# Optimization experiments

Measured on AMD Instinct MI355X. Metric: run time of the kernel, lower is better.

The kernel has to match this reference:

```python
import jax, jax.numpy as jnp
import numpy as np

B, D, E, H, DEPTH, NH, K = 4, 384, 8, 1536, 12, 6, 2
P, NTOK = 16, 197  # patch size, 14*14 patches + cls
EPS = 1e-6


def layernorm(x, w, b):
    m = x.mean(-1, keepdims=True)
    v = ((x - m) ** 2).mean(-1, keepdims=True)
    return (x - m) / jnp.sqrt(v + EPS) * w + b


def attention(x, qkv_w, qkv_b, proj_w, proj_b):
    Bn, N, C = x.shape
    hd = C // NH
    qkv = x @ qkv_w.T + qkv_b                       # [B,N,3C]
    qkv = qkv.reshape(Bn, N, 3, NH, hd).transpose(2, 0, 3, 1, 4)
    q, k, v = qkv[0], qkv[1], qkv[2]                # [B,h,N,hd]
    attn = jax.nn.softmax((q @ k.transpose(0, 1, 3, 2)) * (hd ** -0.5), axis=-1)
    out = (attn @ v).transpose(0, 2, 1, 3).reshape(Bn, N, C)
    return out @ proj_w.T + proj_b


def mlp(x, w1, b1, w2, b2):
    h = jax.nn.gelu(x @ w1.T + b1, approximate=False)
    return h @ w2.T + b2


def moe_ffn(x2d, gw, w1, b1, w2, b2):
    # noiseless top-k gating (eval mode of NoisyTopKGating)
    logits = x2d @ gw                                # [T,E]
    T = logits.shape[0]
    top_vals, top_idx = jax.lax.top_k(logits, K + 1)
    gates_k = jax.nn.softmax(top_vals[:, :K], axis=-1)
    gates = jnp.zeros((T, E), x2d.dtype).at[jnp.arange(T)[:, None], top_idx[:, :K]].set(gates_k)
    # dense per-expert FFN, weighted combine (identical math to SparseDispatcher)
    h = jax.nn.gelu(jnp.einsum('td,edh->teh', x2d, w1) + b1, approximate=False)
    out = jnp.einsum('teh,ehd->ted', h, w2) + b2
    return jnp.einsum('te,ted->td', gates, out)


def forward(x, patch_w, patch_b, cls_token, pos_embed,
            ln1_w, ln1_b, qkv_w, qkv_b, proj_w, proj_b, ln2_w, ln2_b,
            fc1_w, fc1_b, fc2_w, fc2_b,
            gate_w, moe_w1, moe_b1, moe_w2, moe_b2, lnf_w, lnf_b):
    # patch embed: conv k=16 s=16
    feat = jax.lax.conv_general_dilated(x, patch_w, (P, P), 'VALID',
                                        dimension_numbers=('NCHW', 'OIHW', 'NCHW'))
    feat = feat + patch_b[None, :, None, None]
    Bn = feat.shape[0]
    tokens = feat.reshape(Bn, D, -1).transpose(0, 2, 1)          # [B,196,D]
    cls = jnp.broadcast_to(cls_token, (Bn, 1, D))
    h = jnp.concatenate([cls, tokens], axis=1) + pos_embed       # [B,197,D]

    for i in range(DEPTH):
        h = h + attention(layernorm(h, ln1_w[i], ln1_b[i]), qkv_w[i], qkv_b[i], proj_w[i], proj_b[i])
        y = layernorm(h, ln2_w[i], ln2_b[i])
        if i % 2 == 1:
            j = i // 2
            y2 = moe_ffn(y.reshape(-1, D), gate_w[j], moe_w1[j], moe_b1[j], moe_w2[j], moe_b2[j])
            h = h + y2.reshape(Bn, NTOK, D)
        else:
            j = i // 2
            h = h + mlp(y, fc1_w[j], fc1_b[j], fc2_w[j], fc2_b[j])
    return layernorm(h, lnf_w, lnf_b)


def setup_inputs() -> dict:
    key = jax.random.key(0)
    ks = jax.random.split(key, 16)
    rn = lambda k, s, sd=0.02: jax.random.normal(k, s, jnp.float32) * sd
    return {
        'x': jax.random.normal(ks[0], (B, 3, 224, 224), jnp.float32),
        'patch_w': rn(ks[1], (D, 3, P, P)), 'patch_b': jnp.zeros((D,), jnp.float32),
        'cls_token': rn(ks[2], (1, 1, D)), 'pos_embed': rn(ks[3], (1, NTOK, D)),
        'ln1_w': jnp.ones((DEPTH, D), jnp.float32), 'ln1_b': jnp.zeros((DEPTH, D), jnp.float32),
        'qkv_w': rn(ks[4], (DEPTH, 3 * D, D)), 'qkv_b': jnp.zeros((DEPTH, 3 * D), jnp.float32),
        'proj_w': rn(ks[5], (DEPTH, D, D)), 'proj_b': jnp.zeros((DEPTH, D), jnp.float32),
        'ln2_w': jnp.ones((DEPTH, D), jnp.float32), 'ln2_b': jnp.zeros((DEPTH, D), jnp.float32),
        'fc1_w': rn(ks[6], (DEPTH // 2, H, D)), 'fc1_b': jnp.zeros((DEPTH // 2, H), jnp.float32),
        'fc2_w': rn(ks[7], (DEPTH // 2, D, H)), 'fc2_b': jnp.zeros((DEPTH // 2, D), jnp.float32),
        'gate_w': rn(ks[8], (DEPTH // 2, D, E)),
        'moe_w1': rn(ks[9], (DEPTH // 2, E, D, H)), 'moe_b1': jnp.zeros((DEPTH // 2, E, H), jnp.float32),
        'moe_w2': rn(ks[10], (DEPTH // 2, E, H, D)), 'moe_b2': jnp.zeros((DEPTH // 2, E, D), jnp.float32),
        'lnf_w': jnp.ones((D,), jnp.float32), 'lnf_b': jnp.zeros((D,), jnp.float32),
    }


def reference(x, patch_w, patch_b, cls_token, pos_embed,
              ln1_w, ln1_b, qkv_w, qkv_b, proj_w, proj_b, ln2_w, ln2_b,
              fc1_w, fc1_b, fc2_w, fc2_b,
              gate_w, moe_w1, moe_b1, moe_w2, moe_b2, lnf_w, lnf_b):
    return forward(x, patch_w, patch_b, cls_token, pos_embed,
                   ln1_w, ln1_b, qkv_w, qkv_b, proj_w, proj_b, ln2_w, ln2_b,
                   fc1_w, fc1_b, fc2_w, fc2_b,
                   gate_w, moe_w1, moe_b1, moe_w2, moe_b2, lnf_w, lnf_b)
```

## Files before the change

### kernel.cpp

```cpp
#include <hip/hip_runtime.h>
#include <math.h>

#define NBATCH 4
#define NTOK 197
#define TT 788
#define DM 384
#define HM 1536
#define NHEAD 6
#define NEXP 8
#define LD2 72

typedef __attribute__((ext_vector_type(8))) short bf16x8;
typedef __attribute__((ext_vector_type(4))) float f32x4;

__device__ __forceinline__ void f2bf2(float x, short& hi, short& lo) {
    unsigned u = __float_as_uint(x);
    unsigned uh = u + (0x7fffu + ((u >> 16) & 1u));
    hi = (short)(uh >> 16);
    float hf = __uint_as_float(uh & 0xffff0000u);
    float r = x - hf;
    unsigned v = __float_as_uint(r);
    lo = (short)((v + (0x7fffu + ((v >> 16) & 1u))) >> 16);
}
__device__ __forceinline__ float gelu_f(float x) {
    return 0.5f * x * (1.0f + erff(x * 0.7071067811865475f));
}

__global__ void k_ln(const float* __restrict__ X, const float* __restrict__ w,
                     const float* __restrict__ b, float* __restrict__ Y) {
    int t = blockIdx.x, lane = threadIdx.x;
    const float* x = X + (size_t)t * DM;
    float v[6];
    float s = 0.f;
    #pragma unroll
    for (int i = 0; i < 6; ++i) { v[i] = x[lane + i * 64]; s += v[i]; }
    #pragma unroll
    for (int off = 32; off; off >>= 1) s += __shfl_xor(s, off);
    float mean = s * (1.f / 384.f);
    float q = 0.f;
    #pragma unroll
    for (int i = 0; i < 6; ++i) { float d = v[i] - mean; q += d * d; }
    #pragma unroll
    for (int off = 32; off; off >>= 1) q += __shfl_xor(q, off);
    float inv = rsqrtf(q * (1.f / 384.f) + 1e-6f);
    float* y = Y + (size_t)t * DM;
    #pragma unroll
    for (int i = 0; i < 6; ++i) {
        int d = lane + i * 64;
        y[d] = (v[i] - mean) * inv * w[d] + b[d];
    }
}

__global__ __launch_bounds__(256) void k_patch_gemm(
    const float* __restrict__ X, const float* __restrict__ W,
    const float* __restrict__ pb, const float* __restrict__ cls,
    const float* __restrict__ pos, float* __restrict__ H)
{
    const int M = 784, N = 384, K = 768, MT = 13, NT = 6;
    int mt, nt;
    {
        int lane8 = blockIdx.x & 7;
        int idx = blockIdx.x >> 3;
        nt = idx % NT;
        mt = lane8 + 8 * (idx / NT);
        if (mt >= MT) return;
    }
    __shared__ short Ah[64 * LD2], Al[64 * LD2], Bh[64 * LD2], Bl[64 * LD2];
    const int bm = mt * 64, bn = nt * 64;
    const int tid = threadIdx.x;
    const int lane = tid & 63, w = tid >> 6;
    const int wr = w >> 1, wc = w & 1;
    const int r16 = lane & 15, g = lane >> 4;
    const int sr = tid >> 4;
    const int sc = (tid & 15) * 4;
    const float* cvb[4];
    bool aok[4];
    #pragma unroll
    for (int p = 0; p < 4; ++p) {
        int row = bm + sr + p * 16;
        aok[p] = row < M;
        int b = row / 196, pp = row % 196;
        int py = pp / 14, px = pp % 14;
        cvb[p] = X + (size_t)b * 150528 + (size_t)(py * 16) * 224 + px * 16;
    }
    float4 ra[4], rb[4];
    auto LOADT = [&](int k0) {
        int k = k0 + sc;
        int c = k >> 8, ii = (k >> 4) & 15, j = k & 15;
        size_t coff = (size_t)c * 50176 + ii * 224 + j;
        #pragma unroll
        for (int p = 0; p < 4; ++p) {
            ra[p] = aok[p] ? *(const float4*)(cvb[p] + coff) : make_float4(0.f, 0.f, 0.f, 0.f);
            rb[p] = *(const float4*)(W + (size_t)(bn + sr + p * 16) * K + k0 + sc);
        }
    };
    auto STORET = [&]() {
        #pragma unroll
        for (int p = 0; p < 4; ++p) {
            int r = sr + p * 16;
            float4 a4 = ra[p], b4 = rb[p];
            short4 ah, al, bh, bl;
            f2bf2(a4.x, ah.x, al.x); f2bf2(a4.y, ah.y, al.y);
            f2bf2(a4.z, ah.z, al.z); f2bf2(a4.w, ah.w, al.w);
            f2bf2(b4.x, bh.x, bl.x); f2bf2(b4.y, bh.y, bl.y);
            f2bf2(b4.z, bh.z, bl.z); f2bf2(b4.w, bh.w, bl.w);
            *(short4*)&Ah[r * LD2 + sc] = ah; *(short4*)&Al[r * LD2 + sc] = al;
            *(short4*)&Bh[r * LD2 + sc] = bh; *(short4*)&Bl[r * LD2 + sc] = bl;
        }
    };
    f32x4 acc[2][2] = {};
    auto COMPUTE = [&]() {
        #pragma unroll
        for (int kk = 0; kk < 2; ++kk) {
            bf16x8 afh[2], afl[2], bfh[2], bfl[2];
            #pragma unroll
            for (int i = 0; i < 2; ++i) {
                int off = (wr * 32 + i * 16 + r16) * LD2 + kk * 32 + g * 8;
                afh[i] = *(const bf16x8*)&Ah[off];
                afl[i] = *(const bf16x8*)&Al[off];
            }
            #pragma unroll
            for (int j = 0; j < 2; ++j) {
                int off = (wc * 32 + j * 16 + r16) * LD2 + kk * 32 + g * 8;
                bfh[j] = *(const bf16x8*)&Bh[off];
                bfl[j] = *(const bf16x8*)&Bl[off];
            }
            #pragma unroll
            for (int i = 0; i < 2; ++i)
                #pragma unroll
                for (int j = 0; j < 2; ++j) {
                    acc[i][j] = __builtin_amdgcn_mfma_f32_16x16x32_bf16(afl[i], bfh[j], acc[i][j], 0, 0, 0);
                    acc[i][j] = __builtin_amdgcn_mfma_f32_16x16x32_bf16(afh[i], bfl[j], acc[i][j], 0, 0, 0);
                    acc[i][j] = __builtin_amdgcn_mfma_f32_16x16x32_bf16(afh[i], bfh[j], acc[i][j], 0, 0, 0);
                }
        }
    };
    LOADT(0);
    STORET();
    __syncthreads();
    for (int k0 = 64; k0 < K; k0 += 64) {
        LOADT(k0);
        COMPUTE();
        __syncthreads();
        STORET();
        __syncthreads();
    }
    COMPUTE();
    #pragma unroll
    for (int i = 0; i < 2; ++i) {
        #pragma unroll
        for (int j = 0; j < 2; ++j) {
            int n = bn + wc * 32 + j * 16 + r16;
            int mbase = bm + wr * 32 + i * 16 + g * 4;
            #pragma unroll
            for (int r = 0; r < 4; ++r) {
                int m = mbase + r;
                if (m < M) {
                    int b = m / 196, pp = m % 196;
                    int t = b * NTOK + 1 + pp;
                    H[(size_t)t * DM + n] = acc[i][j][r] + pb[n] + pos[(size_t)(1 + pp) * DM + n];
                }
            }
        }
    }
    if (blockIdx.x == 0) {
        for (int idx = tid; idx < NBATCH * DM; idx += 256) {
            int b = idx / DM, d = idx % DM;
            H[(size_t)(b * NTOK) * DM + d] = cls[d] + pos[d];
        }
    }
}

__global__ __launch_bounds__(256) void k_gemm_mfma(
    const float* __restrict__ A, const float* __restrict__ W,
    const float* __restrict__ bias, float* __restrict__ C,
    int M, int N, int K, int flags, int MT, int NT, int wprot, int ksplit,
    const float* __restrict__ lnw, const float* __restrict__ lnb)
{
    int mt, nt, ks = 0;
    {
        int lane8 = blockIdx.x & 7;
        int idx = blockIdx.x >> 3;
        if (ksplit > 1) { ks = idx % ksplit; idx /= ksplit; }
        if (wprot) {
            mt = idx % MT;
            nt = lane8 + 8 * (idx / MT);
            if (nt >= NT) return;
        } else {
            nt = idx % NT;
            mt = lane8 + 8 * (idx / NT);
            if (mt >= MT) return;
        }
    }
    const int Ks = K / ksplit;
    const float* Ab = A + (size_t)ks * Ks;
    const float* Wb = W + (size_t)ks * Ks;
    __shared__ short Ah[64 * LD2], Al[64 * LD2], Bh[64 * LD2], Bl[64 * LD2];
    const int bm = mt * 64, bn = nt * 64;
    const int tid = threadIdx.x;
    const int lane = tid & 63, w = tid >> 6;
    const int wr = w >> 1, wc = w & 1;
    const int r16 = lane & 15, g = lane >> 4;
    const int sr = tid >> 4;
    const int sc = (tid & 15) * 4;
    const bool doln = (flags & 8) != 0;
    float am[4], ai[4];
    #pragma unroll
    for (int p = 0; p < 4; ++p) { am[p] = 0.f; ai[p] = 1.f; }
    if (doln) {
        int j = tid & 15;
        #pragma unroll
        for (int p = 0; p < 4; ++p) {
            int r = bm + sr + p * 16;
            if (r < M) {
                const float* xr = A + (size_t)r * K;
                float s = 0.f, ss = 0.f;
                #pragma unroll
                for (int i = 0; i < 6; ++i) {
                    float4 v = *(const float4*)(xr + j * 4 + i * 64);
                    s += v.x + v.y + v.z + v.w;
                    ss += v.x * v.x + v.y * v.y + v.z * v.z + v.w * v.w;
                }
                #pragma unroll
                for (int off = 1; off < 16; off <<= 1) {
                    s += __shfl_xor(s, off);
                    ss += __shfl_xor(ss, off);
                }
                float mean = s * (1.f / 384.f);
                float var = ss * (1.f / 384.f) - mean * mean;
                am[p] = mean;
                ai[p] = rsqrtf(var + 1e-6f);
            }
        }
    }
    float4 ra[4], rb[4], lw4, lb4;
    auto LOADT = [&](int k0) {
        if (doln) {
            lw4 = *(const float4*)(lnw + k0 + sc);
            lb4 = *(const float4*)(lnb + k0 + sc);
        }
        #pragma unroll
        for (int p = 0; p < 4; ++p) {
            int r = sr + p * 16;
            ra[p] = make_float4(0.f, 0.f, 0.f, 0.f);
            if (bm + r < M) ra[p] = *(const float4*)(Ab + (size_t)(bm + r) * K + k0 + sc);
            rb[p] = *(const float4*)(Wb + (size_t)(bn + r) * K + k0 + sc);
        }
    };
    auto STORET = [&]() {
        #pragma unroll
        for (int p = 0; p < 4; ++p) {
            int r = sr + p * 16;
            float4 a4 = ra[p];
            if (doln) {
                a4.x = (a4.x - am[p]) * ai[p] * lw4.x + lb4.x;
                a4.y = (a4.y - am[p]) * ai[p] * lw4.y + lb4.y;
                a4.z = (a4.z - am[p]) * ai[p] * lw4.z + lb4.z;
                a4.w = (a4.w - am[p]) * ai[p] * lw4.w + lb4.w;
            }
            float4 b4 = rb[p];
            short4 ah, al, bh, bl;
            f2bf2(a4.x, ah.x, al.x); f2bf2(a4.y, ah.y, al.y);
            f2bf2(a4.z, ah.z, al.z); f2bf2(a4.w, ah.w, al.w);
            f2bf2(b4.x, bh.x, bl.x); f2bf2(b4.y, bh.y, bl.y);
            f2bf2(b4.z, bh.z, bl.z); f2bf2(b4.w, bh.w, bl.w);
            *(short4*)&Ah[r * LD2 + sc] = ah; *(short4*)&Al[r * LD2 + sc] = al;
            *(short4*)&Bh[r * LD2 + sc] = bh; *(short4*)&Bl[r * LD2 + sc] = bl;
        }
    };
    f32x4 acc[2][2] = {};
    auto COMPUTE = [&]() {
        #pragma unroll
        for (int kk = 0; kk < 2; ++kk) {
            bf16x8 afh[2], afl[2], bfh[2], bfl[2];
            #pragma unroll
            for (int i = 0; i < 2; ++i) {
                int off = (wr * 32 + i * 16 + r16) * LD2 + kk * 32 + g * 8;
                afh[i] = *(const bf16x8*)&Ah[off];
                afl[i] = *(const bf16x8*)&Al[off];
            }
            #pragma unroll
            for (int j = 0; j < 2; ++j) {
                int off = (wc * 32 + j * 16 + r16) * LD2 + kk * 32 + g * 8;
                bfh[j] = *(const bf16x8*)&Bh[off];
                bfl[j] = *(const bf16x8*)&Bl[off];
            }
            #pragma unroll
            for (int i = 0; i < 2; ++i)
                #pragma unroll
                for (int j = 0; j < 2; ++j) {
                    acc[i][j] = __builtin_amdgcn_mfma_f32_16x16x32_bf16(afl[i], bfh[j], acc[i][j], 0, 0, 0);
                    acc[i][j] = __builtin_amdgcn_mfma_f32_16x16x32_bf16(afh[i], bfl[j], acc[i][j], 0, 0, 0);
                    acc[i][j] = __builtin_amdgcn_mfma_f32_16x16x32_bf16(afh[i], bfh[j], acc[i][j], 0, 0, 0);
                }
        }
    };
    LOADT(0);
    STORET();
    __syncthreads();
    for (int k0 = 64; k0 < Ks; k0 += 64) {
        LOADT(k0);
        COMPUTE();
        __syncthreads();
        STORET();
        __syncthreads();
    }
    COMPUTE();
    #pragma unroll
    for (int i = 0; i < 2; ++i) {
        #pragma unroll
        for (int j = 0; j < 2; ++j) {
            int n = bn + wc * 32 + j * 16 + r16;
            float bb = (bias && ks == 0) ? bias[n] : 0.f;
            int mbase = bm + wr * 32 + i * 16 + g * 4;
            #pragma unroll
            for (int r = 0; r < 4; ++r) {
                int m = mbase + r;
                if (m < M) {
                    float v = acc[i][j][r] + bb;
                    float* cp = C + (size_t)m * N + n;
                    if (flags & 16) {
                        atomicAdd(cp, v);
                    } else {
                        if (flags & 1) v = gelu_f(v);
                        if (flags & 2) v += *cp;
                        *cp = v;
                    }
                }
            }
        }
    }
}

__global__ __launch_bounds__(256) void k_scoresm(const float* __restrict__ QKV,
                                                 float* __restrict__ S) {
    int z = blockIdx.y;
    int b = z / NHEAD, hh = z % NHEAD;
    int i0 = blockIdx.x * 32;
    __shared__ float qs[32][65];
    __shared__ float ks[32][65];
    __shared__ float srow[32][200];
    int tid = threadIdx.x;
    int r = tid >> 3, d0 = (tid & 7) * 8, c0 = (tid & 7) * 4, l8 = tid & 7;
    {
        float4 v0 = make_float4(0,0,0,0), v1 = v0;
        if (i0 + r < NTOK) {
            const float* qp = QKV + ((size_t)(b * NTOK + i0 + r)) * 1152 + hh * 64 + d0;
            v0 = *(const float4*)qp; v1 = *(const float4*)(qp + 4);
        }
        qs[r][d0+0]=v0.x; qs[r][d0+1]=v0.y; qs[r][d0+2]=v0.z; qs[r][d0+3]=v0.w;
        qs[r][d0+4]=v1.x; qs[r][d0+5]=v1.y; qs[r][d0+6]=v1.z; qs[r][d0+7]=v1.w;
    }
    if (l8 == 0) { srow[r][197] = -1e30f; srow[r][198] = -1e30f; srow[r][199] = -1e30f; }
    for (int j0 = 0; j0 < NTOK; j0 += 32) {
        __syncthreads();
        {
            float4 v0 = make_float4(0,0,0,0), v1 = v0;
            if (j0 + r < NTOK) {
                const float* kp = QKV + ((size_t)(b * NTOK + j0 + r)) * 1152 + 384 + hh * 64 + d0;
                v0 = *(const float4*)kp; v1 = *(const float4*)(kp + 4);
            }
            ks[r][d0+0]=v0.x; ks[r][d0+1]=v0.y; ks[r][d0+2]=v0.z; ks[r][d0+3]=v0.w;
            ks[r][d0+4]=v1.x; ks[r][d0+5]=v1.y; ks[r][d0+6]=v1.z; ks[r][d0+7]=v1.w;
        }
        __syncthreads();
        float acc[4] = {0.f, 0.f, 0.f, 0.f};
        #pragma unroll 8
        for (int d = 0; d < 64; ++d) {
            float qv = qs[r][d];
            #pragma unroll
            for (int u = 0; u < 4; ++u) acc[u] += qv * ks[c0 + u][d];
        }
        #pragma unroll
        for (int u = 0; u < 4; ++u) {
            int j = j0 + c0 + u;
            if (j < NTOK) srow[r][j] = acc[u] * 0.125f;
        }
    }
    __syncthreads();
    float m = -1e30f;
    for (int c = l8; c < 200; c += 8) m = fmaxf(m, srow[r][c]);
    #pragma unroll
    for (int off = 1; off < 8; off <<= 1) m = fmaxf(m, __shfl_xor(m, off));
    float s = 0.f;
    for (int c = l8; c < 200; c += 8) {
        float e = expf(srow[r][c] - m);
        srow[r][c] = e;
        s += e;
    }
    #pragma unroll
    for (int off = 1; off < 8; off <<= 1) s += __shfl_xor(s, off);
    float invs = 1.f / s;
    int i = i0 + r;
    if (i < NTOK) {
        float* sp = S + ((size_t)z * NTOK + i) * NTOK;
        for (int c = l8; c < NTOK; c += 8) sp[c] = srow[r][c] * invs;
    }
}

__global__ __launch_bounds__(256) void k_pv(const float* __restrict__ S, const float* __restrict__ QKV,
                                            float* __restrict__ AO) {
    int z = blockIdx.y;
    int b = z / NHEAD, hh = z % NHEAD;
    int i0 = blockIdx.x * 32;
    __shared__ float ps[32][33];
    __shared__ float vs[32][65];
    int tid = threadIdx.x;
    int r = tid >> 3;
    int c4 = (tid & 7) * 4;
    int d0 = (tid & 7) * 8;
    float acc[8] = {};
    for (int k0 = 0; k0 < NTOK; k0 += 32) {
        #pragma unroll
        for (int u = 0; u < 4; ++u) {
            int i = i0 + r, j = k0 + c4 + u;
            ps[r][c4 + u] = (i < NTOK && j < NTOK) ? S[((size_t)z * NTOK + i) * NTOK + j] : 0.f;
        }
        {
            float4 v0 = make_float4(0,0,0,0), v1 = v0;
            if (k0 + r < NTOK) {
                const float* vp = QKV + ((size_t)(b * NTOK + k0 + r)) * 1152 + 768 + hh * 64 + d0;
                v0 = *(const float4*)vp; v1 = *(const float4*)(vp + 4);
            }
            vs[r][d0+0]=v0.x; vs[r][d0+1]=v0.y; vs[r][d0+2]=v0.z; vs[r][d0+3]=v0.w;
            vs[r][d0+4]=v1.x; vs[r][d0+5]=v1.y; vs[r][d0+6]=v1.z; vs[r][d0+7]=v1.w;
        }
        __syncthreads();
        #pragma unroll 8
        for (int kk = 0; kk < 32; ++kk) {
            float pw = ps[r][kk];
            #pragma unroll
            for (int j = 0; j < 8; ++j) acc[j] += pw * vs[kk][d0 + j];
        }
        __syncthreads();
    }
    int i = i0 + r;
    if (i < NTOK) {
        float* op = AO + (size_t)(b * NTOK + i) * DM + hh * 64 + d0;
        #pragma unroll
        for (int j = 0; j < 8; ++j) op[j] = acc[j];
    }
}

__global__ void k_route_ln(const float* __restrict__ H, float* __restrict__ lnstat,
                           const float* __restrict__ lnw, const float* __restrict__ lnb,
                           const float* __restrict__ GW,
                           int* __restrict__ eidx, float* __restrict__ egate) {
    int t = blockIdx.x * 4 + (threadIdx.x >> 6);
    if (t >= TT) return;
    int lane = threadIdx.x & 63;
    const float* x = H + (size_t)t * DM;
    float v[6];
    float s = 0.f, ss = 0.f;
    #pragma unroll
    for (int i = 0; i < 6; ++i) {
        v[i] = x[lane + i * 64];
        s += v[i];
        ss += v[i] * v[i];
    }
    #pragma unroll
    for (int off = 32; off; off >>= 1) { s += __shfl_xor(s, off); ss += __shfl_xor(ss, off); }
    float mean = s * (1.f / 384.f);
    float var = ss * (1.f / 384.f) - mean * mean;
    float inv = rsqrtf(var + 1e-6f);
    if (lane == 0) { lnstat[2 * t] = mean; lnstat[2 * t + 1] = inv; }
    float l8v[NEXP] = {};
    #pragma unroll
    for (int i = 0; i < 6; ++i) {
        int d = lane + i * 64;
        float yv = (v[i] - mean) * inv * lnw[d] + lnb[d];
        const float* g = GW + (size_t)d * NEXP;
        #pragma unroll
        for (int e = 0; e < NEXP; ++e) l8v[e] += yv * g[e];
    }
    #pragma unroll
    for (int e = 0; e < NEXP; ++e) {
        float vv = l8v[e];
        #pragma unroll
        for (int off = 32; off; off >>= 1) vv += __shfl_xor(vv, off);
        l8v[e] = vv;
    }
    if (lane == 0) {
        int b0 = 0;
        #pragma unroll
        for (int e = 1; e < NEXP; ++e) if (l8v[e] > l8v[b0]) b0 = e;
        int b1 = -1;
        #pragma unroll
        for (int e = 0; e < NEXP; ++e) if (e != b0 && (b1 < 0 || l8v[e] > l8v[b1])) b1 = e;
        float e1 = expf(l8v[b1] - l8v[b0]);
        float denom = 1.f + e1;
        eidx[2 * t] = b0; eidx[2 * t + 1] = b1;
        egate[2 * t] = 1.f / denom; egate[2 * t + 1] = e1 / denom;
    }
}

__global__ void k_pscatter(int* __restrict__ cnt, int* __restrict__ basep,
                           const int* __restrict__ eidx, const float* __restrict__ egate,
                           int* __restrict__ slot_tok, float* __restrict__ slot_gate) {
    __shared__ int hist[NEXP];
    __shared__ int bp[NEXP];
    __shared__ int fl[NEXP];
    int tid = threadIdx.x;
    if (tid < NEXP) { hist[tid] = 0; fl[tid] = 0; }
    __syncthreads();
    for (int i = tid; i < 2 * TT; i += 256) atomicAdd(&hist[eidx[i]], 1);
    __syncthreads();
    if (tid == 0) {
        int s = 0;
        for (int e = 0; e < NEXP; ++e) { bp[e] = s; s += hist[e]; }
    }
    __syncthreads();
    if (tid < NEXP) { cnt[tid] = hist[tid]; basep[tid] = bp[tid]; }
    for (int t = tid; t < TT; t += 256) {
        #pragma unroll
        for (int k = 0; k < 2; ++k) {
            int e = eidx[2 * t + k];
            int pos = atomicAdd(&fl[e], 1);
            int s = bp[e] + pos;
            slot_tok[s] = t;
            slot_gate[s] = egate[2 * t + k];
        }
    }
}

__global__ __launch_bounds__(256) void k_moe1_mfma(
    const float* __restrict__ H, const float* __restrict__ lnstat,
    const float* __restrict__ lnw, const float* __restrict__ lnb,
    const float* __restrict__ W1, const float* __restrict__ B1,
    const int* __restrict__ slot_tok, const int* __restrict__ cnt, const int* __restrict__ basep,
    float* __restrict__ HID)
{
    const int e = blockIdx.x & 7;
    const int idx = blockIdx.x >> 3;
    const int mt = idx % 13;
    const int nt = idx / 13;
    const int c = cnt[e];
    const int r0 = mt * 64;
    if (r0 >= c) return;
    const int sbase = basep[e];
    const int n0 = nt * 64;
    const float* W = W1 + (size_t)e * DM * HM;
    const float* B1e = B1 + (size_t)e * HM;
    __shared__ short Ah[64 * LD2], Al[64 * LD2], Bh[64 * LD2], Bl[64 * LD2];
    const int tid = threadIdx.x;
    const int lane = tid & 63, w = tid >> 6;
    const int wr = w >> 1, wc = w & 1;
    const int r16 = lane & 15, g = lane >> 4;
    const int sr = tid >> 4, sc = (tid & 15) * 4;
    const int kq = (tid >> 4) * 4;
    int tokp[4];
    float am4[4], ai4[4];
    #pragma unroll
    for (int p = 0; p < 4; ++p) {
        int m = r0 + sr + p * 16;
        tokp[p] = (m < c) ? slot_tok[sbase + m] : -1;
        am4[p] = 0.f; ai4[p] = 1.f;
        if (tokp[p] >= 0) { am4[p] = lnstat[2 * tokp[p]]; ai4[p] = lnstat[2 * tokp[p] + 1]; }
    }
    f32x4 acc[2][2] = {};
    for (int k0 = 0; k0 < DM; k0 += 64) {
        float4 lw4 = *(const float4*)(lnw + k0 + sc);
        float4 lb4 = *(const float4*)(lnb + k0 + sc);
        #pragma unroll
        for (int p = 0; p < 4; ++p) {
            int r = sr + p * 16;
            float4 a4 = make_float4(0.f, 0.f, 0.f, 0.f);
            if (tokp[p] >= 0) {
                a4 = *(const float4*)(H + (size_t)tokp[p] * DM + k0 + sc);
                a4.x = (a4.x - am4[p]) * ai4[p] * lw4.x + lb4.x;
                a4.y = (a4.y - am4[p]) * ai4[p] * lw4.y + lb4.y;
                a4.z = (a4.z - am4[p]) * ai4[p] * lw4.z + lb4.z;
                a4.w = (a4.w - am4[p]) * ai4[p] * lw4.w + lb4.w;
            }
            short4 ah, al;
            f2bf2(a4.x, ah.x, al.x); f2bf2(a4.y, ah.y, al.y);
            f2bf2(a4.z, ah.z, al.z); f2bf2(a4.w, ah.w, al.w);
            *(short4*)&Ah[r * LD2 + sc] = ah; *(short4*)&Al[r * LD2 + sc] = al;
        }
        {
            float4 b4[4];
            #pragma unroll
            for (int i = 0; i < 4; ++i)
                b4[i] = *(const float4*)(W + (size_t)(k0 + kq + i) * HM + n0 + sc);
            float col[4][4] = {
                { b4[0].x, b4[1].x, b4[2].x, b4[3].x },
                { b4[0].y, b4[1].y, b4[2].y, b4[3].y },
                { b4[0].z, b4[1].z, b4[2].z, b4[3].z },
                { b4[0].w, b4[1].w, b4[2].w, b4[3].w } };
            #pragma unroll
            for (int u = 0; u < 4; ++u) {
                short4 hh, ll;
                f2bf2(col[u][0], hh.x, ll.x); f2bf2(col[u][1], hh.y, ll.y);
                f2bf2(col[u][2], hh.z, ll.z); f2bf2(col[u][3], hh.w, ll.w);
                *(short4*)&Bh[(sc + u) * LD2 + kq] = hh;
                *(short4*)&Bl[(sc + u) * LD2 + kq] = ll;
            }
        }
        __syncthreads();
        #pragma unroll
        for (int kk = 0; kk < 2; ++kk) {
            bf16x8 afh[2], afl[2], bfh[2], bfl[2];
            #pragma unroll
            for (int i = 0; i < 2; ++i) {
                int off = (wr * 32 + i * 16 + r16) * LD2 + kk * 32 + g * 8;
                afh[i] = *(const bf16x8*)&Ah[off];
                afl[i] = *(const bf16x8*)&Al[off];
            }
            #pragma unroll
            for (int j = 0; j < 2; ++j) {
                int off = (wc * 32 + j * 16 + r16) * LD2 + kk * 32 + g * 8;
                bfh[j] = *(const bf16x8*)&Bh[off];
                bfl[j] = *(const bf16x8*)&Bl[off];
            }
            #pragma unroll
            for (int i = 0; i < 2; ++i)
                #pragma unroll
                for (int j = 0; j < 2; ++j) {
                    acc[i][j] = __builtin_amdgcn_mfma_f32_16x16x32_bf16(afl[i], bfh[j], acc[i][j], 0, 0, 0);
                    acc[i][j] = __builtin_amdgcn_mfma_f32_16x16x32_bf16(afh[i], bfl[j], acc[i][j], 0, 0, 0);
                    acc[i][j] = __builtin_amdgcn_mfma_f32_16x16x32_bf16(afh[i], bfh[j], acc[i][j], 0, 0, 0);
                }
        }
        __syncthreads();
    }
    #pragma unroll
    for (int i = 0; i < 2; ++i) {
        #pragma unroll
        for (int j = 0; j < 2; ++j) {
            int n = n0 + wc * 32 + j * 16 + r16;
            float bb = B1e[n];
            #pragma unroll
            for (int r = 0; r < 4; ++r) {
                int m = r0 + wr * 32 + i * 16 + g * 4 + r;
                if (m < c)
                    HID[(size_t)(sbase + m) * HM + n] = gelu_f(acc[i][j][r] + bb);
            }
        }
    }
}

__global__ __launch_bounds__(256) void k_moe2_mfma(
    const float* __restrict__ HID, const float* __restrict__ W2, const float* __restrict__ B2,
    const int* __restrict__ cnt, const int* __restrict__ basep,
    const int* __restrict__ slot_tok, const float* __restrict__ slot_gate,
    float* __restrict__ H)
{
    const int e = blockIdx.x & 7;
    const int idx = blockIdx.x >> 3;
    const int mt = idx % 13;
    const int rest = idx / 13;
    const int nt = rest % 6;
    const int ks = rest / 6;
    const int c = cnt[e];
    const int r0 = mt * 64;
    if (r0 >= c) return;
    const int sbase = basep[e];
    const int n0 = nt * 64;
    const int kbase = ks * 384;
    const float* W = W2 + (size_t)e * HM * DM + (size_t)kbase * DM;
    const float* B2e = B2 + (size_t)e * DM;
    __shared__ short Ah[64 * LD2], Al[64 * LD2], Bh[64 * LD2], Bl[64 * LD2];
    const int tid = threadIdx.x;
    const int lane = tid & 63, w = tid >> 6;
    const int wr = w >> 1, wc = w & 1;
    const int r16 = lane & 15, g = lane >> 4;
    const int sr = tid >> 4, sc = (tid & 15) * 4;
    const int kq = (tid >> 4) * 4;
    f32x4 acc[2][2] = {};
    for (int k0 = 0; k0 < 384; k0 += 64) {
        #pragma unroll
        for (int p = 0; p < 4; ++p) {
            int r = sr + p * 16;
            int m = r0 + r;
            float4 a4 = make_float4(0.f, 0.f, 0.f, 0.f);
            if (m < c) a4 = *(const float4*)(HID + (size_t)(sbase + m) * HM + kbase + k0 + sc);
            short4 ah, al;
            f2bf2(a4.x, ah.x, al.x); f2bf2(a4.y, ah.y, al.y);
            f2bf2(a4.z, ah.z, al.z); f2bf2(a4.w, ah.w, al.w);
            *(short4*)&Ah[r * LD2 + sc] = ah; *(short4*)&Al[r * LD2 + sc] = al;
        }
        {
            float4 b4[4];
            #pragma unroll
            for (int i = 0; i < 4; ++i)
                b4[i] = *(const float4*)(W + (size_t)(k0 + kq + i) * DM + n0 + sc);
            float col[4][4] = {
                { b4[0].x, b4[1].x, b4[2].x, b4[3].x },
                { b4[0].y, b4[1].y, b4[2].y, b4[3].y },
                { b4[0].z, b4[1].z, b4[2].z, b4[3].z },
                { b4[0].w, b4[1].w, b4[2].w, b4[3].w } };
            #pragma unroll
            for (int u = 0; u < 4; ++u) {
                short4 hh, ll;
                f2bf2(col[u][0], hh.x, ll.x); f2bf2(col[u][1], hh.y, ll.y);
                f2bf2(col[u][2], hh.z, ll.z); f2bf2(col[u][3], hh.w, ll.w);
                *(short4*)&Bh[(sc + u) * LD2 + kq] = hh;
                *(short4*)&Bl[(sc + u) * LD2 + kq] = ll;
            }
        }
        __syncthreads();
        #pragma unroll
        for (int kk = 0; kk < 2; ++kk) {
            bf16x8 afh[2], afl[2], bfh[2], bfl[2];
            #pragma unroll
            for (int i = 0; i < 2; ++i) {
                int off = (wr * 32 + i * 16 + r16) * LD2 + kk * 32 + g * 8;
                afh[i] = *(const bf16x8*)&Ah[off];
                afl[i] = *(const bf16x8*)&Al[off];
            }
            #pragma unroll
            for (int j = 0; j < 2; ++j) {
                int off = (wc * 32 + j * 16 + r16) * LD2 + kk * 32 + g * 8;
                bfh[j] = *(const bf16x8*)&Bh[off];
                bfl[j] = *(const bf16x8*)&Bl[off];
            }
            #pragma unroll
            for (int i = 0; i < 2; ++i)
                #pragma unroll
                for (int j = 0; j < 2; ++j) {
                    acc[i][j] = __builtin_amdgcn_mfma_f32_16x16x32_bf16(afl[i], bfh[j], acc[i][j], 0, 0, 0);
                    acc[i][j] = __builtin_amdgcn_mfma_f32_16x16x32_bf16(afh[i], bfl[j], acc[i][j], 0, 0, 0);
                    acc[i][j] = __builtin_amdgcn_mfma_f32_16x16x32_bf16(afh[i], bfh[j], acc[i][j], 0, 0, 0);
                }
        }
        __syncthreads();
    }
    #pragma unroll
    for (int i = 0; i < 2; ++i) {
        #pragma unroll
        for (int j = 0; j < 2; ++j) {
            int n = n0 + wc * 32 + j * 16 + r16;
            float bb = (ks == 0) ? B2e[n] : 0.f;
            #pragma unroll
            for (int r = 0; r < 4; ++r) {
                int m = r0 + wr * 32 + i * 16 + g * 4 + r;
                if (m < c) {
                    int tok = slot_tok[sbase + m];
                    float gt = slot_gate[sbase + m];
                    atomicAdd(&H[(size_t)tok * DM + n], gt * (acc[i][j][r] + bb));
                }
            }
        }
    }
}

extern "C" void kernel_launch(void* const* d_in, const int* in_sizes, int n_in,
                              void* d_out, int out_size, void* d_ws, size_t ws_size,
                              hipStream_t stream) {
    const float* x         = (const float*)d_in[0];
    const float* patch_w   = (const float*)d_in[1];
    const float* patch_b   = (const float*)d_in[2];
    const float* cls_token = (const float*)d_in[3];
    const float* pos_embed = (const float*)d_in[4];
    const float* ln1_w     = (const float*)d_in[5];
    const float* ln1_b     = (const float*)d_in[6];
    const float* qkv_w     = (const float*)d_in[7];
    const float* qkv_b     = (const float*)d_in[8];
    const float* proj_w    = (const float*)d_in[9];
    const float* proj_b    = (const float*)d_in[10];
    const float* ln2_w     = (const float*)d_in[11];
    const float* ln2_b     = (const float*)d_in[12];
    const float* fc1_w     = (const float*)d_in[13];
    const float* fc1_b     = (const float*)d_in[14];
    const float* fc2_w     = (const float*)d_in[15];
    const float* fc2_b     = (const float*)d_in[16];
    const float* gate_w    = (const float*)d_in[17];
    const float* moe_w1    = (const float*)d_in[18];
    const float* moe_b1    = (const float*)d_in[19];
    const float* moe_w2    = (const float*)d_in[20];
    const float* moe_b2    = (const float*)d_in[21];
    const float* lnf_w     = (const float*)d_in[22];
    const float* lnf_b     = (const float*)d_in[23];
    float* out = (float*)d_out;

    float* wsf = (float*)d_ws;
    float* regA     = wsf;
    float* moehid   = regA;
    float* h     = regA + 2420736;
    float* spare = h + 302592;
    float* qkvb  = spare + 302592;
    float* attno = qkvb + 907776;
    float* regC  = attno + 302592;
    float* S    = regC;
    float* hid  = regC;
    float* egate = regC + 1210368;
    int* ib       = (int*)(egate + 1576);
    int* eidx     = ib;
    int* slot_tok = ib + 1576;
    int* slot_of  = ib + 3152;
    int* cnt      = ib + 4728;
    int* basep    = ib + 4736;
    float* lnstat = (float*)(ib + 4752);
    float* slot_gate = lnstat + 1576;

    k_patch_gemm<<<96, 256, 0, stream>>>(x, patch_w, patch_b, cls_token, pos_embed, h);

    for (int l = 0; l < 12; ++l) {
        k_gemm_mfma<<<312, 256, 0, stream>>>(h, qkv_w + (size_t)l * 1152 * DM,
                                             qkv_b + l * 1152, qkvb, TT, 1152, DM, 8,
                                             13, 18, 1, 1,
                                             ln1_w + l * DM, ln1_b + l * DM);
        k_scoresm<<<dim3(7, NBATCH * NHEAD), 256, 0, stream>>>(qkvb, S);
        k_pv<<<dim3(7, NBATCH * NHEAD), 256, 0, stream>>>(S, qkvb, attno);
        k_gemm_mfma<<<192, 256, 0, stream>>>(attno, proj_w + (size_t)l * DM * DM,
                                             proj_b + l * DM, h, TT, DM, DM, 16,
                                             13, 6, 0, 2, nullptr, nullptr);
        int j = l >> 1;
        if ((l & 1) == 0) {
            k_gemm_mfma<<<312, 256, 0, stream>>>(h, fc1_w + (size_t)j * HM * DM,
                                                 fc1_b + j * HM, hid, TT, HM, DM, 9,
                                                 13, 24, 1, 1,
                                                 ln2_w + l * DM, ln2_b + l * DM);
            k_gemm_mfma<<<384, 256, 0, stream>>>(hid, fc2_w + (size_t)j * DM * HM,
                                                 fc2_b + j * DM, h, TT, DM, HM, 16,
                                                 13, 6, 0, 4, nullptr, nullptr);
        } else {
            k_route_ln<<<197, 256, 0, stream>>>(h, lnstat, ln2_w + l * DM, ln2_b + l * DM,
                                                gate_w + (size_t)j * DM * NEXP, eidx, egate);
            k_pscatter<<<1, 256, 0, stream>>>(cnt, basep, eidx, egate, slot_tok, slot_gate);
            k_moe1_mfma<<<8 * 13 * 24, 256, 0, stream>>>(
                h, lnstat, ln2_w + l * DM, ln2_b + l * DM,
                moe_w1 + (size_t)j * NEXP * DM * HM, moe_b1 + (size_t)j * NEXP * HM,
                slot_tok, cnt, basep, moehid);
            k_moe2_mfma<<<8 * 13 * 24, 256, 0, stream>>>(
                moehid, moe_w2 + (size_t)j * NEXP * HM * DM, moe_b2 + (size_t)j * NEXP * DM,
                cnt, basep, slot_tok, slot_gate, h);
        }
    }
    k_ln<<<TT, 64, 0, stream>>>(h, lnf_w, lnf_b, out);
}
```

Baseline: 1.681 ms.

## Fuse whole ViT-MoE forward into one persistent cooperative megakernel

Replaces the sequence of roughly 70 separate kernel launches with a single cooperative persistent kernel. The former kernels become device functions looped over virtual block indices, with grid-wide syncs between stages. This removes per-launch overhead and inter-kernel gaps, but costs a grid barrier per stage and caps the grid at 512 blocks, so large stages like the MoE GEMMs run in several waves. It also moves the fc1 GELU from the fc1 epilogue into the fc2 A-operand load path, so GELU is recomputed for each output tile that reads hid.

```diff
diff --git a/kernel.cpp b/kernel.cpp
--- a/kernel.cpp
+++ b/kernel.cpp
@@ -1,5 +1,8 @@
 #include <hip/hip_runtime.h>
+#include <hip/hip_cooperative_groups.h>
 #include <math.h>
+
+namespace cg = cooperative_groups;
 
 #define NBATCH 4
 #define NTOK 197
@@ -26,161 +29,27 @@
     return 0.5f * x * (1.0f + erff(x * 0.7071067811865475f));
 }
 
-__global__ void k_ln(const float* __restrict__ X, const float* __restrict__ w,
-                     const float* __restrict__ b, float* __restrict__ Y) {
-    int t = blockIdx.x, lane = threadIdx.x;
-    const float* x = X + (size_t)t * DM;
-    float v[6];
-    float s = 0.f;
-    #pragma unroll
-    for (int i = 0; i < 6; ++i) { v[i] = x[lane + i * 64]; s += v[i]; }
-    #pragma unroll
-    for (int off = 32; off; off >>= 1) s += __shfl_xor(s, off);
-    float mean = s * (1.f / 384.f);
-    float q = 0.f;
-    #pragma unroll
-    for (int i = 0; i < 6; ++i) { float d = v[i] - mean; q += d * d; }
-    #pragma unroll
-    for (int off = 32; off; off >>= 1) q += __shfl_xor(q, off);
-    float inv = rsqrtf(q * (1.f / 384.f) + 1e-6f);
-    float* y = Y + (size_t)t * DM;
-    #pragma unroll
-    for (int i = 0; i < 6; ++i) {
-        int d = lane + i * 64;
-        y[d] = (v[i] - mean) * inv * w[d] + b[d];
-    }
-}
-
-__global__ __launch_bounds__(256) void k_patch_gemm(
-    const float* __restrict__ X, const float* __restrict__ W,
-    const float* __restrict__ pb, const float* __restrict__ cls,
-    const float* __restrict__ pos, float* __restrict__ H)
-{
-    const int M = 784, N = 384, K = 768, MT = 13, NT = 6;
-    int mt, nt;
-    {
-        int lane8 = blockIdx.x & 7;
-        int idx = blockIdx.x >> 3;
-        nt = idx % NT;
-        mt = lane8 + 8 * (idx / NT);
-        if (mt >= MT) return;
-    }
-    __shared__ short Ah[64 * LD2], Al[64 * LD2], Bh[64 * LD2], Bl[64 * LD2];
-    const int bm = mt * 64, bn = nt * 64;
-    const int tid = threadIdx.x;
-    const int lane = tid & 63, w = tid >> 6;
-    const int wr = w >> 1, wc = w & 1;
-    const int r16 = lane & 15, g = lane >> 4;
-    const int sr = tid >> 4;
-    const int sc = (tid & 15) * 4;
-    const float* cvb[4];
-    bool aok[4];
-    #pragma unroll
-    for (int p = 0; p < 4; ++p) {
-        int row = bm + sr + p * 16;
-        aok[p] = row < M;
-        int b = row / 196, pp = row % 196;
-        int py = pp / 14, px = pp % 14;
-        cvb[p] = X + (size_t)b * 150528 + (size_t)(py * 16) * 224 + px * 16;
-    }
-    float4 ra[4], rb[4];
-    auto LOADT = [&](int k0) {
-        int k = k0 + sc;
-        int c = k >> 8, ii = (k >> 4) & 15, j = k & 15;
-        size_t coff = (size_t)c * 50176 + ii * 224 + j;
-        #pragma unroll
-        for (int p = 0; p < 4; ++p) {
-            ra[p] = aok[p] ? *(const float4*)(cvb[p] + coff) : make_float4(0.f, 0.f, 0.f, 0.f);
-            rb[p] = *(const float4*)(W + (size_t)(bn + sr + p * 16) * K + k0 + sc);
-        }
-    };
-    auto STORET = [&]() {
-        #pragma unroll
-        for (int p = 0; p < 4; ++p) {
-            int r = sr + p * 16;
-            float4 a4 = ra[p], b4 = rb[p];
-            short4 ah, al, bh, bl;
-            f2bf2(a4.x, ah.x, al.x); f2bf2(a4.y, ah.y, al.y);
-            f2bf2(a4.z, ah.z, al.z); f2bf2(a4.w, ah.w, al.w);
-            f2bf2(b4.x, bh.x, bl.x); f2bf2(b4.y, bh.y, bl.y);
-            f2bf2(b4.z, bh.z, bl.z); f2bf2(b4.w, bh.w, bl.w);
-            *(short4*)&Ah[r * LD2 + sc] = ah; *(short4*)&Al[r * LD2 + sc] = al;
-            *(short4*)&Bh[r * LD2 + sc] = bh; *(short4*)&Bl[r * LD2 + sc] = bl;
-        }
-    };
-    f32x4 acc[2][2] = {};
-    auto COMPUTE = [&]() {
-        #pragma unroll
-        for (int kk = 0; kk < 2; ++kk) {
-            bf16x8 afh[2], afl[2], bfh[2], bfl[2];
-            #pragma unroll
-            for (int i = 0; i < 2; ++i) {
-                int off = (wr * 32 + i * 16 + r16) * LD2 + kk * 32 + g * 8;
-                afh[i] = *(const bf16x8*)&Ah[off];
-                afl[i] = *(const bf16x8*)&Al[off];
-            }
-            #pragma unroll
-            for (int j = 0; j < 2; ++j) {
-                int off = (wc * 32 + j * 16 + r16) * LD2 + kk * 32 + g * 8;
-                bfh[j] = *(const bf16x8*)&Bh[off];
-                bfl[j] = *(const bf16x8*)&Bl[off];
-            }
-            #pragma unroll
-            for (int i = 0; i < 2; ++i)
-                #pragma unroll
-                for (int j = 0; j < 2; ++j) {
-                    acc[i][j] = __builtin_amdgcn_mfma_f32_16x16x32_bf16(afl[i], bfh[j], acc[i][j], 0, 0, 0);
-                    acc[i][j] = __builtin_amdgcn_mfma_f32_16x16x32_bf16(afh[i], bfl[j], acc[i][j], 0, 0, 0);
-                    acc[i][j] = __builtin_amdgcn_mfma_f32_16x16x32_bf16(afh[i], bfh[j], acc[i][j], 0, 0, 0);
-                }
-        }
-    };
-    LOADT(0);
-    STORET();
-    __syncthreads();
-    for (int k0 = 64; k0 < K; k0 += 64) {
-        LOADT(k0);
-        COMPUTE();
-        __syncthreads();
-        STORET();
-        __syncthreads();
-    }
-    COMPUTE();
-    #pragma unroll
-    for (int i = 0; i < 2; ++i) {
-        #pragma unroll
-        for (int j = 0; j < 2; ++j) {
-            int n = bn + wc * 32 + j * 16 + r16;
-            int mbase = bm + wr * 32 + i * 16 + g * 4;
-            #pragma unroll
-            for (int r = 0; r < 4; ++r) {
-                int m = mbase + r;
-                if (m < M) {
-                    int b = m / 196, pp = m % 196;
-                    int t = b * NTOK + 1 + pp;
-                    H[(size_t)t * DM + n] = acc[i][j][r] + pb[n] + pos[(size_t)(1 + pp) * DM + n];
-                }
-            }
-        }
-    }
-    if (blockIdx.x == 0) {
-        for (int idx = tid; idx < NBATCH * DM; idx += 256) {
-            int b = idx / DM, d = idx % DM;
-            H[(size_t)(b * NTOK) * DM + d] = cls[d] + pos[d];
-        }
-    }
-}
-
-__global__ __launch_bounds__(256) void k_gemm_mfma(
-    const float* __restrict__ A, const float* __restrict__ W,
-    const float* __restrict__ bias, float* __restrict__ C,
-    int M, int N, int K, int flags, int MT, int NT, int wprot, int ksplit,
-    const float* __restrict__ lnw, const float* __restrict__ lnb)
+struct MParams {
+    const float *x, *patch_w, *patch_b, *cls_token, *pos_embed;
+    const float *ln1_w, *ln1_b, *qkv_w, *qkv_b, *proj_w, *proj_b;
+    const float *ln2_w, *ln2_b, *fc1_w, *fc1_b, *fc2_w, *fc2_b;
+    const float *gate_w, *moe_w1, *moe_b1, *moe_w2, *moe_b2;
+    const float *lnf_w, *lnf_b;
+    float *out;
+    float *h, *qkvb, *attno, *S, *hid, *moehid;
+    float *egate, *lnstat, *slot_gate;
+    int *eidx, *slot_tok, *cnt, *basep;
+};
+
+__device__ void gemm_dev(int vb, float* smem,
+                         const float* A, const float* W, const float* bias, float* C,
+                         int M, int N, int K, int flags, int MT, int NT, int wprot, int ksplit,
+                         const float* lnw, const float* lnb)
 {
     int mt, nt, ks = 0;
     {
-        int lane8 = blockIdx.x & 7;
-        int idx = blockIdx.x >> 3;
+        int lane8 = vb & 7;
+        int idx = vb >> 3;
         if (ksplit > 1) { ks = idx % ksplit; idx /= ksplit; }
         if (wprot) {
             mt = idx % MT;
@@ -195,7 +64,10 @@
     const int Ks = K / ksplit;
     const float* Ab = A + (size_t)ks * Ks;
     const float* Wb = W + (size_t)ks * Ks;
-    __shared__ short Ah[64 * LD2], Al[64 * LD2], Bh[64 * LD2], Bl[64 * LD2];
+    short* Ah = (short*)smem;
+    short* Al = Ah + 64 * LD2;
+    short* Bh = Al + 64 * LD2;
+    short* Bl = Bh + 64 * LD2;
     const int bm = mt * 64, bn = nt * 64;
     const int tid = threadIdx.x;
     const int lane = tid & 63, w = tid >> 6;
@@ -204,6 +76,7 @@
     const int sr = tid >> 4;
     const int sc = (tid & 15) * 4;
     const bool doln = (flags & 8) != 0;
+    const bool dogelu_a = (flags & 32) != 0;
     float am[4], ai[4];
     #pragma unroll
     for (int p = 0; p < 4; ++p) { am[p] = 0.f; ai[p] = 1.f; }
@@ -252,6 +125,10 @@
         for (int p = 0; p < 4; ++p) {
             int r = sr + p * 16;
             float4 a4 = ra[p];
+            if (dogelu_a) {
+                a4.x = gelu_f(a4.x); a4.y = gelu_f(a4.y);
+                a4.z = gelu_f(a4.z); a4.w = gelu_f(a4.w);
+            }
             if (doln) {
                 a4.x = (a4.x - am[p]) * ai[p] * lw4.x + lb4.x;
                 a4.y = (a4.y - am[p]) * ai[p] * lw4.y + lb4.y;
@@ -319,27 +196,155 @@
                 if (m < M) {
                     float v = acc[i][j][r] + bb;
                     float* cp = C + (size_t)m * N + n;
-                    if (flags & 16) {
-                        atomicAdd(cp, v);
-                    } else {
-                        if (flags & 1) v = gelu_f(v);
-                        if (flags & 2) v += *cp;
-                        *cp = v;
-                    }
+                    if (flags & 16) atomicAdd(cp, v);
+                    else *cp = v;
                 }
             }
         }
     }
 }
 
-__global__ __launch_bounds__(256) void k_scoresm(const float* __restrict__ QKV,
-                                                 float* __restrict__ S) {
-    int z = blockIdx.y;
+__device__ void patch_dev(int vb, float* smem,
+                          const float* X, const float* W, const float* pb,
+                          const float* cls, const float* pos, float* H)
+{
+    const int M = 784, K = 768, NT = 6;
+    int mt, nt;
+    {
+        int lane8 = vb & 7;
+        int idx = vb >> 3;
+        nt = idx % NT;
+        mt = lane8 + 8 * (idx / NT);
+    }
+    const int tid = threadIdx.x;
+    if (vb == 0) {
+    }
+    if (mt >= 13) {
+        if (vb == 0) {
+            for (int idx2 = tid; idx2 < NBATCH * DM; idx2 += 256) {
+                int b = idx2 / DM, d = idx2 % DM;
+                H[(size_t)(b * NTOK) * DM + d] = cls[d] + pos[d];
+            }
+        }
+        return;
+    }
+    short* Ah = (short*)smem;
+    short* Al = Ah + 64 * LD2;
+    short* Bh = Al + 64 * LD2;
+    short* Bl = Bh + 64 * LD2;
+    const int bm = mt * 64, bn = nt * 64;
+    const int lane = tid & 63, w = tid >> 6;
+    const int wr = w >> 1, wc = w & 1;
+    const int r16 = lane & 15, g = lane >> 4;
+    const int sr = tid >> 4;
+    const int sc = (tid & 15) * 4;
+    const float* cvb[4];
+    bool aok[4];
+    #pragma unroll
+    for (int p = 0; p < 4; ++p) {
+        int row = bm + sr + p * 16;
+        aok[p] = row < M;
+        int b = row / 196, pp = row % 196;
+        int py = pp / 14, px = pp % 14;
+        cvb[p] = X + (size_t)b * 150528 + (size_t)(py * 16) * 224 + px * 16;
+    }
+    float4 ra[4], rb[4];
+    auto LOADT = [&](int k0) {
+        int k = k0 + sc;
+        int c = k >> 8, ii = (k >> 4) & 15, j = k & 15;
+        size_t coff = (size_t)c * 50176 + ii * 224 + j;
+        #pragma unroll
+        for (int p = 0; p < 4; ++p) {
+            ra[p] = aok[p] ? *(const float4*)(cvb[p] + coff) : make_float4(0.f, 0.f, 0.f, 0.f);
+            rb[p] = *(const float4*)(W + (size_t)(bn + sr + p * 16) * K + k0 + sc);
+        }
+    };
+    auto STORET = [&]() {
+        #pragma unroll
+        for (int p = 0; p < 4; ++p) {
+            int r = sr + p * 16;
+            float4 a4 = ra[p], b4 = rb[p];
+            short4 ah, al, bh, bl;
+            f2bf2(a4.x, ah.x, al.x); f2bf2(a4.y, ah.y, al.y);
+            f2bf2(a4.z, ah.z, al.z); f2bf2(a4.w, ah.w, al.w);
+            f2bf2(b4.x, bh.x, bl.x); f2bf2(b4.y, bh.y, bl.y);
+            f2bf2(b4.z, bh.z, bl.z); f2bf2(b4.w, bh.w, bl.w);
+            *(short4*)&Ah[r * LD2 + sc] = ah; *(short4*)&Al[r * LD2 + sc] = al;
+            *(short4*)&Bh[r * LD2 + sc] = bh; *(short4*)&Bl[r * LD2 + sc] = bl;
+        }
+    };
+    f32x4 acc[2][2] = {};
+    auto COMPUTE = [&]() {
+        #pragma unroll
+        for (int kk = 0; kk < 2; ++kk) {
+            bf16x8 afh[2], afl[2], bfh[2], bfl[2];
+            #pragma unroll
+            for (int i = 0; i < 2; ++i) {
+                int off = (wr * 32 + i * 16 + r16) * LD2 + kk * 32 + g * 8;
+                afh[i] = *(const bf16x8*)&Ah[off];
+                afl[i] = *(const bf16x8*)&Al[off];
+            }
+            #pragma unroll
+            for (int j = 0; j < 2; ++j) {
+                int off = (wc * 32 + j * 16 + r16) * LD2 + kk * 32 + g * 8;
+                bfh[j] = *(const bf16x8*)&Bh[off];
+                bfl[j] = *(const bf16x8*)&Bl[off];
+            }
+            #pragma unroll
+            for (int i = 0; i < 2; ++i)
+                #pragma unroll
+                for (int j = 0; j < 2; ++j) {
+                    acc[i][j] = __builtin_amdgcn_mfma_f32_16x16x32_bf16(afl[i], bfh[j], acc[i][j], 0, 0, 0);
+                    acc[i][j] = __builtin_amdgcn_mfma_f32_16x16x32_bf16(afh[i], bfl[j], acc[i][j], 0, 0, 0);
+                    acc[i][j] = __builtin_amdgcn_mfma_f32_16x16x32_bf16(afh[i], bfh[j], acc[i][j], 0, 0, 0);
+                }
+        }
+    };
+    LOADT(0);
+    STORET();
+    __syncthreads();
+    for (int k0 = 64; k0 < K; k0 += 64) {
+        LOADT(k0);
+        COMPUTE();
+        __syncthreads();
+        STORET();
+        __syncthreads();
+    }
+    COMPUTE();
+    #pragma unroll
+    for (int i = 0; i < 2; ++i) {
+        #pragma unroll
+        for (int j = 0; j < 2; ++j) {
+            int n = bn + wc * 32 + j * 16 + r16;
+            int mbase = bm + wr * 32 + i * 16 + g * 4;
+            #pragma unroll
+            for (int r = 0; r < 4; ++r) {
+                int m = mbase + r;
+                if (m < M) {
+                    int b = m / 196, pp = m % 196;
+                    int t = b * NTOK + 1 + pp;
+                    H[(size_t)t * DM + n] = acc[i][j][r] + pb[n] + pos[(size_t)(1 + pp) * DM + n];
+                }
+            }
+        }
+    }
+    if (vb == 0) {
+        for (int idx2 = tid; idx2 < NBATCH * DM; idx2 += 256) {
+            int b = idx2 / DM, d = idx2 % DM;
+            H[(size_t)(b * NTOK) * DM + d] = cls[d] + pos[d];
+        }
+    }
+}
+
+__device__ void scoresm_dev(int vb, float* smem,
+                            const float* QKV, float* S)
+{
+    int z = vb / 7;
+    int i0 = (vb % 7) * 32;
     int b = z / NHEAD, hh = z % NHEAD;
-    int i0 = blockIdx.x * 32;
-    __shared__ float qs[32][65];
-    __shared__ float ks[32][65];
-    __shared__ float srow[32][200];
+    float* qs = smem;
+    float* ks = smem + 2080;
+    float* srow = smem + 4160;
     int tid = threadIdx.x;
     int r = tid >> 3, d0 = (tid & 7) * 8, c0 = (tid & 7) * 4, l8 = tid & 7;
     {
@@ -348,10 +353,13 @@
             const float* qp = QKV + ((size_t)(b * NTOK + i0 + r)) * 1152 + hh * 64 + d0;
             v0 = *(const float4*)qp; v1 = *(const float4*)(qp + 4);
         }
-        qs[r][d0+0]=v0.x; qs[r][d0+1]=v0.y; qs[r][d0+2]=v0.z; qs[r][d0+3]=v0.w;
-        qs[r][d0+4]=v1.x; qs[r][d0+5]=v1.y; qs[r][d0+6]=v1.z; qs[r][d0+7]=v1.w;
-    }
-    if (l8 == 0) { srow[r][197] = -1e30f; srow[r][198] = -1e30f; srow[r][199] = -1e30f; }
+        float* q = qs + r * 65 + d0;
+        q[0]=v0.x; q[1]=v0.y; q[2]=v0.z; q[3]=v0.w;
+        q[4]=v1.x; q[5]=v1.y; q[6]=v1.z; q[7]=v1.w;
+    }
+    if (l8 == 0) {
+        srow[r * 200 + 197] = -1e30f; srow[r * 200 + 198] = -1e30f; srow[r * 200 + 199] = -1e30f;
+    }
     for (int j0 = 0; j0 < NTOK; j0 += 32) {
         __syncthreads();
         {
@@ -360,32 +368,33 @@
                 const float* kp = QKV + ((size_t)(b * NTOK + j0 + r)) * 1152 + 384 + hh * 64 + d0;
                 v0 = *(const float4*)kp; v1 = *(const float4*)(kp + 4);
             }
-            ks[r][d0+0]=v0.x; ks[r][d0+1]=v0.y; ks[r][d0+2]=v0.z; ks[r][d0+3]=v0.w;
-            ks[r][d0+4]=v1.x; ks[r][d0+5]=v1.y; ks[r][d0+6]=v1.z; ks[r][d0+7]=v1.w;
+            float* k = ks + r * 65 + d0;
+            k[0]=v0.x; k[1]=v0.y; k[2]=v0.z; k[3]=v0.w;
+            k[4]=v1.x; k[5]=v1.y; k[6]=v1.z; k[7]=v1.w;
         }
         __syncthreads();
         float acc[4] = {0.f, 0.f, 0.f, 0.f};
         #pragma unroll 8
         for (int d = 0; d < 64; ++d) {
-            float qv = qs[r][d];
-            #pragma unroll
-            for (int u = 0; u < 4; ++u) acc[u] += qv * ks[c0 + u][d];
+            float qv = qs[r * 65 + d];
+            #pragma unroll
+            for (int u = 0; u < 4; ++u) acc[u] += qv * ks[(c0 + u) * 65 + d];
         }
         #pragma unroll
         for (int u = 0; u < 4; ++u) {
             int j = j0 + c0 + u;
-            if (j < NTOK) srow[r][j] = acc[u] * 0.125f;
+            if (j < NTOK) srow[r * 200 + j] = acc[u] * 0.125f;
         }
     }
     __syncthreads();
     float m = -1e30f;
-    for (int c = l8; c < 200; c += 8) m = fmaxf(m, srow[r][c]);
+    for (int c = l8; c < 200; c += 8) m = fmaxf(m, srow[r * 200 + c]);
     #pragma unroll
     for (int off = 1; off < 8; off <<= 1) m = fmaxf(m, __shfl_xor(m, off));
     float s = 0.f;
     for (int c = l8; c < 200; c += 8) {
-        float e = expf(srow[r][c] - m);
-        srow[r][c] = e;
+        float e = expf(srow[r * 200 + c] - m);
+        srow[r * 200 + c] = e;
         s += e;
     }
     #pragma unroll
@@ -394,17 +403,18 @@
     int i = i0 + r;
     if (i < NTOK) {
         float* sp = S + ((size_t)z * NTOK + i) * NTOK;
-        for (int c = l8; c < NTOK; c += 8) sp[c] = srow[r][c] * invs;
-    }
-}
-
-__global__ __launch_bounds__(256) void k_pv(const float* __restrict__ S, const float* __restrict__ QKV,
-                                            float* __restrict__ AO) {
-    int z = blockIdx.y;
+        for (int c = l8; c < NTOK; c += 8) sp[c] = srow[r * 200 + c] * invs;
+    }
+}
+
+__device__ void pv_dev(int vb, float* smem,
+                       const float* S, const float* QKV, float* AO)
+{
+    int z = vb / 7;
+    int i0 = (vb % 7) * 32;
     int b = z / NHEAD, hh = z % NHEAD;
-    int i0 = blockIdx.x * 32;
-    __shared__ float ps[32][33];
-    __shared__ float vs[32][65];
+    float* ps = smem;
+    float* vs = smem + 1056;
     int tid = threadIdx.x;
     int r = tid >> 3;
     int c4 = (tid & 7) * 4;
@@ -414,7 +424,7 @@
         #pragma unroll
         for (int u = 0; u < 4; ++u) {
             int i = i0 + r, j = k0 + c4 + u;
-            ps[r][c4 + u] = (i < NTOK && j < NTOK) ? S[((size_t)z * NTOK + i) * NTOK + j] : 0.f;
+            ps[r * 33 + c4 + u] = (i < NTOK && j < NTOK) ? S[((size_t)z * NTOK + i) * NTOK + j] : 0.f;
         }
         {
             float4 v0 = make_float4(0,0,0,0), v1 = v0;
@@ -422,15 +432,16 @@
                 const float* vp = QKV + ((size_t)(b * NTOK + k0 + r)) * 1152 + 768 + hh * 64 + d0;
                 v0 = *(const float4*)vp; v1 = *(const float4*)(vp + 4);
             }
-            vs[r][d0+0]=v0.x; vs[r][d0+1]=v0.y; vs[r][d0+2]=v0.z; vs[r][d0+3]=v0.w;
-            vs[r][d0+4]=v1.x; vs[r][d0+5]=v1.y; vs[r][d0+6]=v1.z; vs[r][d0+7]=v1.w;
+            float* v = vs + r * 65 + d0;
+            v[0]=v0.x; v[1]=v0.y; v[2]=v0.z; v[3]=v0.w;
+            v[4]=v1.x; v[5]=v1.y; v[6]=v1.z; v[7]=v1.w;
         }
         __syncthreads();
         #pragma unroll 8
         for (int kk = 0; kk < 32; ++kk) {
-            float pw = ps[r][kk];
-            #pragma unroll
-            for (int j = 0; j < 8; ++j) acc[j] += pw * vs[kk][d0 + j];
+            float pw = ps[r * 33 + kk];
+            #pragma unroll
+            for (int j = 0; j < 8; ++j) acc[j] += pw * vs[kk * 65 + d0 + j];
         }
         __syncthreads();
     }
@@ -442,11 +453,11 @@
     }
 }
 
-__global__ void k_route_ln(const float* __restrict__ H, float* __restrict__ lnstat,
-                           const float* __restrict__ lnw, const float* __restrict__ lnb,
-                           const float* __restrict__ GW,
-                           int* __restrict__ eidx, float* __restrict__ egate) {
-    int t = blockIdx.x * 4 + (threadIdx.x >> 6);
+__device__ void route_dev(int vb, const float* H, float* lnstat,
+                          const float* lnw, const float* lnb, const float* GW,
+                          int* eidx, float* egate)
+{
+    int t = vb * 4 + (threadIdx.x >> 6);
     if (t >= TT) return;
     int lane = threadIdx.x & 63;
     const float* x = H + (size_t)t * DM;
@@ -494,12 +505,13 @@
     }
 }
 
-__global__ void k_pscatter(int* __restrict__ cnt, int* __restrict__ basep,
-                           const int* __restrict__ eidx, const float* __restrict__ egate,
-                           int* __restrict__ slot_tok, float* __restrict__ slot_gate) {
-    __shared__ int hist[NEXP];
-    __shared__ int bp[NEXP];
-    __shared__ int fl[NEXP];
+__device__ void pscatter_dev(float* smem, int* cnt, int* basep,
+                             const int* eidx, const float* egate,
+                             int* slot_tok, float* slot_gate)
+{
+    int* hist = (int*)smem;
+    int* bp = hist + NEXP;
+    int* fl = bp + NEXP;
     int tid = threadIdx.x;
     if (tid < NEXP) { hist[tid] = 0; fl[tid] = 0; }
     __syncthreads();
@@ -523,15 +535,15 @@
     }
 }
 
-__global__ __launch_bounds__(256) void k_moe1_mfma(
-    const float* __restrict__ H, const float* __restrict__ lnstat,
-    const float* __restrict__ lnw, const float* __restrict__ lnb,
-    const float* __restrict__ W1, const float* __restrict__ B1,
-    const int* __restrict__ slot_tok, const int* __restrict__ cnt, const int* __restrict__ basep,
-    float* __restrict__ HID)
+__device__ void moe1_dev(int vb, float* smem,
+                         const float* H, const float* lnstat,
+                         const float* lnw, const float* lnb,
+                         const float* W1, const float* B1,
+                         const int* slot_tok, const int* cnt, const int* basep,
+                         float* HID)
 {
-    const int e = blockIdx.x & 7;
-    const int idx = blockIdx.x >> 3;
+    const int e = vb & 7;
+    const int idx = vb >> 3;
     const int mt = idx % 13;
     const int nt = idx / 13;
     const int c = cnt[e];
@@ -541,7 +553,10 @@
     const int n0 = nt * 64;
     const float* W = W1 + (size_t)e * DM * HM;
     const float* B1e = B1 + (size_t)e * HM;
-    __shared__ short Ah[64 * LD2], Al[64 * LD2], Bh[64 * LD2], Bl[64 * LD2];
+    short* Ah = (short*)smem;
+    short* Al = Ah + 64 * LD2;
+    short* Bh = Al + 64 * LD2;
+    short* Bl = Bh + 64 * LD2;
     const int tid = threadIdx.x;
     const int lane = tid & 63, w = tid >> 6;
     const int wr = w >> 1, wc = w & 1;
@@ -639,14 +654,14 @@
     }
 }
 
-__global__ __launch_bounds__(256) void k_moe2_mfma(
-    const float* __restrict__ HID, const float* __restrict__ W2, const float* __restrict__ B2,
-    const int* __restrict__ cnt, const int* __restrict__ basep,
-    const int* __restrict__ slot_tok, const float* __restrict__ slot_gate,
-    float* __restrict__ H)
+__device__ void moe2_dev(int vb, float* smem,
+                         const float* HID, const float* W2, const float* B2,
+                         const int* cnt, const int* basep,
+                         const int* slot_tok, const float* slot_gate,
+                         float* H)
 {
-    const int e = blockIdx.x & 7;
-    const int idx = blockIdx.x >> 3;
+    const int e = vb & 7;
+    const int idx = vb >> 3;
     const int mt = idx % 13;
     const int rest = idx / 13;
     const int nt = rest % 6;
@@ -659,7 +674,10 @@
     const int kbase = ks * 384;
     const float* W = W2 + (size_t)e * HM * DM + (size_t)kbase * DM;
     const float* B2e = B2 + (size_t)e * DM;
-    __shared__ short Ah[64 * LD2], Al[64 * LD2], Bh[64 * LD2], Bl[64 * LD2];
+    short* Ah = (short*)smem;
+    short* Al = Ah + 64 * LD2;
+    short* Bh = Al + 64 * LD2;
+    short* Bl = Bh + 64 * LD2;
     const int tid = threadIdx.x;
     const int lane = tid & 63, w = tid >> 6;
     const int wr = w >> 1, wc = w & 1;
@@ -744,88 +762,165 @@
     }
 }
 
+__device__ void lnf_dev(int vb, const float* X, const float* w,
+                        const float* b, float* Y)
+{
+    int t = vb * 4 + (threadIdx.x >> 6);
+    if (t >= TT) return;
+    int lane = threadIdx.x & 63;
+    const float* x = X + (size_t)t * DM;
+    float v[6];
+    float s = 0.f, ss = 0.f;
+    #pragma unroll
+    for (int i = 0; i < 6; ++i) {
+        v[i] = x[lane + i * 64];
+        s += v[i];
+        ss += v[i] * v[i];
+    }
+    #pragma unroll
+    for (int off = 32; off; off >>= 1) { s += __shfl_xor(s, off); ss += __shfl_xor(ss, off); }
+    float mean = s * (1.f / 384.f);
+    float var = ss * (1.f / 384.f) - mean * mean;
+    float inv = rsqrtf(var + 1e-6f);
+    float* y = Y + (size_t)t * DM;
+    #pragma unroll
+    for (int i = 0; i < 6; ++i) {
+        int d = lane + i * 64;
+        y[d] = (v[i] - mean) * inv * w[d] + b[d];
+    }
+}
+
+__global__ void __launch_bounds__(256) k_mega(MParams p) {
+    cg::grid_group gg = cg::this_grid();
+    __shared__ float smem[10560];
+
+    for (int vb = blockIdx.x; vb < 96; vb += gridDim.x) {
+        patch_dev(vb, smem, p.x, p.patch_w, p.patch_b, p.cls_token, p.pos_embed, p.h);
+        __syncthreads();
+    }
+    gg.sync();
+
+    for (int l = 0; l < 12; ++l) {
+        int j = l >> 1;
+        for (int vb = blockIdx.x; vb < 312; vb += gridDim.x) {
+            gemm_dev(vb, smem, p.h, p.qkv_w + (size_t)l * 1152 * DM, p.qkv_b + l * 1152,
+                     p.qkvb, TT, 1152, DM, 8, 13, 18, 1, 1,
+                     p.ln1_w + l * DM, p.ln1_b + l * DM);
+            __syncthreads();
+        }
+        gg.sync();
+        for (int vb = blockIdx.x; vb < 168; vb += gridDim.x) {
+            scoresm_dev(vb, smem, p.qkvb, p.S);
+            __syncthreads();
+        }
+        gg.sync();
+        for (int vb = blockIdx.x; vb < 168; vb += gridDim.x) {
+            pv_dev(vb, smem, p.S, p.qkvb, p.attno);
+            __syncthreads();
+        }
+        gg.sync();
+        for (int vb = blockIdx.x; vb < 192; vb += gridDim.x) {
+            gemm_dev(vb, smem, p.attno, p.proj_w + (size_t)l * DM * DM, p.proj_b + l * DM,
+                     p.h, TT, DM, DM, 16, 13, 6, 0, 2, nullptr, nullptr);
+            __syncthreads();
+        }
+        gg.sync();
+        if ((l & 1) == 0) {
+            for (int vb = blockIdx.x; vb < 312; vb += gridDim.x) {
+                gemm_dev(vb, smem, p.h, p.fc1_w + (size_t)j * HM * DM, p.fc1_b + j * HM,
+                         p.hid, TT, HM, DM, 8, 13, 24, 1, 1,
+                         p.ln2_w + l * DM, p.ln2_b + l * DM);
+                __syncthreads();
+            }
+            gg.sync();
+            for (int vb = blockIdx.x; vb < 384; vb += gridDim.x) {
+                gemm_dev(vb, smem, p.hid, p.fc2_w + (size_t)j * DM * HM, p.fc2_b + j * DM,
+                         p.h, TT, DM, HM, 16 | 32, 13, 6, 0, 4, nullptr, nullptr);
+                __syncthreads();
+            }
+            gg.sync();
+        } else {
+            for (int vb = blockIdx.x; vb < 197; vb += gridDim.x)
+                route_dev(vb, p.h, p.lnstat, p.ln2_w + l * DM, p.ln2_b + l * DM,
+                          p.gate_w + (size_t)j * DM * NEXP, p.eidx, p.egate);
+            gg.sync();
+            if (blockIdx.x == 0)
+                pscatter_dev(smem, p.cnt, p.basep, p.eidx, p.egate, p.slot_tok, p.slot_gate);
+            gg.sync();
+            for (int vb = blockIdx.x; vb < 2496; vb += gridDim.x) {
+                moe1_dev(vb, smem, p.h, p.lnstat, p.ln2_w + l * DM, p.ln2_b + l * DM,
+                         p.moe_w1 + (size_t)j * NEXP * DM * HM, p.moe_b1 + (size_t)j * NEXP * HM,
+                         p.slot_tok, p.cnt, p.basep, p.moehid);
+                __syncthreads();
+            }
+            gg.sync();
+            for (int vb = blockIdx.x; vb < 2496; vb += gridDim.x) {
+                moe2_dev(vb, smem, p.moehid, p.moe_w2 + (size_t)j * NEXP * HM * DM,
+                         p.moe_b2 + (size_t)j * NEXP * DM,
+                         p.cnt, p.basep, p.slot_tok, p.slot_gate, p.h);
+                __syncthreads();
+            }
+            gg.sync();
+        }
+    }
+    for (int vb = blockIdx.x; vb < 197; vb += gridDim.x)
+        lnf_dev(vb, p.h, p.lnf_w, p.lnf_b, p.out);
+}
+
 extern "C" void kernel_launch(void* const* d_in, const int* in_sizes, int n_in,
                               void* d_out, int out_size, void* d_ws, size_t ws_size,
                               hipStream_t stream) {
-    const float* x         = (const float*)d_in[0];
-    const float* patch_w   = (const float*)d_in[1];
-    const float* patch_b   = (const float*)d_in[2];
-    const float* cls_token = (const float*)d_in[3];
-    const float* pos_embed = (const float*)d_in[4];
-    const float* ln1_w     = (const float*)d_in[5];
-    const float* ln1_b     = (const float*)d_in[6];
-    const float* qkv_w     = (const float*)d_in[7];
-    const float* qkv_b     = (const float*)d_in[8];
-    const float* proj_w    = (const float*)d_in[9];
-    const float* proj_b    = (const float*)d_in[10];
-    const float* ln2_w     = (const float*)d_in[11];
-    const float* ln2_b     = (const float*)d_in[12];
-    const float* fc1_w     = (const float*)d_in[13];
-    const float* fc1_b     = (const float*)d_in[14];
-    const float* fc2_w     = (const float*)d_in[15];
-    const float* fc2_b     = (const float*)d_in[16];
-    const float* gate_w    = (const float*)d_in[17];
-    const float* moe_w1    = (const float*)d_in[18];
-    const float* moe_b1    = (const float*)d_in[19];
-    const float* moe_w2    = (const float*)d_in[20];
-    const float* moe_b2    = (const float*)d_in[21];
-    const float* lnf_w     = (const float*)d_in[22];
-    const float* lnf_b     = (const float*)d_in[23];
-    float* out = (float*)d_out;
+    MParams p;
+    p.x         = (const float*)d_in[0];
+    p.patch_w   = (const float*)d_in[1];
+    p.patch_b   = (const float*)d_in[2];
+    p.cls_token = (const float*)d_in[3];
+    p.pos_embed = (const float*)d_in[4];
+    p.ln1_w     = (const float*)d_in[5];
+    p.ln1_b     = (const float*)d_in[6];
+    p.qkv_w     = (const float*)d_in[7];
+    p.qkv_b     = (const float*)d_in[8];
+    p.proj_w    = (const float*)d_in[9];
+    p.proj_b    = (const float*)d_in[10];
+    p.ln2_w     = (const float*)d_in[11];
+    p.ln2_b     = (const float*)d_in[12];
+    p.fc1_w     = (const float*)d_in[13];
+    p.fc1_b     = (const float*)d_in[14];
+    p.fc2_w     = (const float*)d_in[15];
+    p.fc2_b     = (const float*)d_in[16];
+    p.gate_w    = (const float*)d_in[17];
+    p.moe_w1    = (const float*)d_in[18];
+    p.moe_b1    = (const float*)d_in[19];
+    p.moe_w2    = (const float*)d_in[20];
+    p.moe_b2    = (const float*)d_in[21];
+    p.lnf_w     = (const float*)d_in[22];
+    p.lnf_b     = (const float*)d_in[23];
+    p.out = (float*)d_out;
 
     float* wsf = (float*)d_ws;
-    float* regA     = wsf;
-    float* moehid   = regA;
-    float* h     = regA + 2420736;
-    float* spare = h + 302592;
-    float* qkvb  = spare + 302592;
-    float* attno = qkvb + 907776;
-    float* regC  = attno + 302592;
-    float* S    = regC;
-    float* hid  = regC;
-    float* egate = regC + 1210368;
-    int* ib       = (int*)(egate + 1576);
-    int* eidx     = ib;
-    int* slot_tok = ib + 1576;
-    int* slot_of  = ib + 3152;
-    int* cnt      = ib + 4728;
-    int* basep    = ib + 4736;
-    float* lnstat = (float*)(ib + 4752);
-    float* slot_gate = lnstat + 1576;
-
-    k_patch_gemm<<<96, 256, 0, stream>>>(x, patch_w, patch_b, cls_token, pos_embed, h);
-
-    for (int l = 0; l < 12; ++l) {
-        k_gemm_mfma<<<312, 256, 0, stream>>>(h, qkv_w + (size_t)l * 1152 * DM,
-                                             qkv_b + l * 1152, qkvb, TT, 1152, DM, 8,
-                                             13, 18, 1, 1,
-                                             ln1_w + l * DM, ln1_b + l * DM);
-        k_scoresm<<<dim3(7, NBATCH * NHEAD), 256, 0, stream>>>(qkvb, S);
-        k_pv<<<dim3(7, NBATCH * NHEAD), 256, 0, stream>>>(S, qkvb, attno);
-        k_gemm_mfma<<<192, 256, 0, stream>>>(attno, proj_w + (size_t)l * DM * DM,
-                                             proj_b + l * DM, h, TT, DM, DM, 16,
-                                             13, 6, 0, 2, nullptr, nullptr);
-        int j = l >> 1;
-        if ((l & 1) == 0) {
-            k_gemm_mfma<<<312, 256, 0, stream>>>(h, fc1_w + (size_t)j * HM * DM,
-                                                 fc1_b + j * HM, hid, TT, HM, DM, 9,
-                                                 13, 24, 1, 1,
-                                                 ln2_w + l * DM, ln2_b + l * DM);
-            k_gemm_mfma<<<384, 256, 0, stream>>>(hid, fc2_w + (size_t)j * DM * HM,
-                                                 fc2_b + j * DM, h, TT, DM, HM, 16,
-                                                 13, 6, 0, 4, nullptr, nullptr);
-        } else {
-            k_route_ln<<<197, 256, 0, stream>>>(h, lnstat, ln2_w + l * DM, ln2_b + l * DM,
-                                                gate_w + (size_t)j * DM * NEXP, eidx, egate);
-            k_pscatter<<<1, 256, 0, stream>>>(cnt, basep, eidx, egate, slot_tok, slot_gate);
-            k_moe1_mfma<<<8 * 13 * 24, 256, 0, stream>>>(
-                h, lnstat, ln2_w + l * DM, ln2_b + l * DM,
-                moe_w1 + (size_t)j * NEXP * DM * HM, moe_b1 + (size_t)j * NEXP * HM,
-                slot_tok, cnt, basep, moehid);
-            k_moe2_mfma<<<8 * 13 * 24, 256, 0, stream>>>(
-                moehid, moe_w2 + (size_t)j * NEXP * HM * DM, moe_b2 + (size_t)j * NEXP * DM,
-                cnt, basep, slot_tok, slot_gate, h);
-        }
-    }
-    k_ln<<<TT, 64, 0, stream>>>(h, lnf_w, lnf_b, out);
-}
+    float* regA = wsf;
+    p.moehid = regA;
+    p.h     = regA + 2420736;
+    float* spare = p.h + 302592;
+    p.qkvb  = spare + 302592;
+    p.attno = p.qkvb + 907776;
+    float* regC = p.attno + 302592;
+    p.S   = regC;
+    p.hid = regC;
+    p.egate = regC + 1210368;
+    int* ib = (int*)(p.egate + 1576);
+    p.eidx     = ib;
+    p.slot_tok = ib + 1576;
+    p.cnt      = ib + 4728;
+    p.basep    = ib + 4736;
+    p.lnstat   = (float*)(ib + 4752);
+    p.slot_gate = p.lnstat + 1576;
+
+    int nb = 0;
+    hipOccupancyMaxActiveBlocksPerMultiprocessor(&nb, k_mega, 256, 0);
+    if (nb < 1) nb = 1;
+    int grid = nb * 256;
+    if (grid > 512) grid = 512;
+    void* args[] = { (void*)&p };
+    hipLaunchCooperativeKernel((void*)k_mega, dim3(grid), dim3(256), args, 0, stream);
+}
```

New measurement: 4.583 ms. 173% more time.
